# Performance work log

Hardware: AMD Instinct MI355X
Metric: run time of the kernel (lower is better)

## Reference

```python
import jax, jax.numpy as jnp
import numpy as np

H = 2048      # hidden_size
NH = 8        # attention heads
HD = 256      # head_dim (== global_head_dim here)
FFN = 4096
PLD = 256     # hidden_size_per_layer_input
LTOT = 30     # num_hidden_layers of the whole model (PLE projection width)
NL = 15       # layers in this chunk (L0..L14)
W = 512       # sliding-window cache length
CTX = 1024    # full-attention cache length
POS = 100     # current decode position (seq_len == 1)
FULL_LAYERS = (4, 14)
EPS = 1e-6


def _rms(x, w):
    return x * jax.lax.rsqrt(jnp.mean(x * x, axis=-1, keepdims=True) + EPS) * (1.0 + w)


def _rot_half(x):
    x1, x2 = jnp.split(x, 2, axis=-1)
    return jnp.concatenate([-x2, x1], axis=-1)


def _rope(x, cos, sin):
    return x * cos + _rot_half(x) * sin


def setup_inputs():
    key = jax.random.key(0)
    ks = jax.random.split(key, 24)
    f = jnp.float32
    def w(k, shape, s=0.02):
        return jax.random.normal(k, shape, f) * s
    inp = {}
    inp["hidden_states"] = jax.random.normal(ks[0], (1, 1, H), f)
    pos = jnp.arange(CTX)
    inp["causal_mask_full"] = jnp.where(pos <= POS, 0.0, -1e9).astype(f).reshape(1, 1, 1, CTX)
    pw = jnp.arange(W)
    inp["causal_mask_sliding"] = jnp.where((pw <= POS) & (pw > POS - W), 0.0, -1e9).astype(f).reshape(1, 1, 1, W)
    inp["update_mask"] = (pos == POS).astype(f).reshape(1, 1, CTX, 1)
    inp["per_layer_raw"] = jax.random.normal(ks[1], (1, 1, LTOT * PLD), f)
    def rope_tab(base):
        inv = 1.0 / (base ** (jnp.arange(0, HD, 2, dtype=f) / HD))
        ang = POS * inv
        c = jnp.concatenate([jnp.cos(ang), jnp.cos(ang)]).reshape(1, 1, 1, HD)
        s = jnp.concatenate([jnp.sin(ang), jnp.sin(ang)]).reshape(1, 1, 1, HD)
        return c, s
    inp["cos_s"], inp["sin_s"] = rope_tab(10000.0)   # local layers rope_theta
    inp["cos_f"], inp["sin_f"] = rope_tab(1000000.0) # global layers rope_theta
    inp["K_sliding_in"] = jax.random.normal(ks[2], (13, 1, W, HD), f)
    inp["V_sliding_in"] = jax.random.normal(ks[3], (13, 1, W, HD), f)
    inp["K_full_in"] = jax.random.normal(ks[4], (2, 1, CTX, HD), f)
    inp["V_full_in"] = jax.random.normal(ks[5], (2, 1, CTX, HD), f)
    # learned parameters, stacked over the NL chunk layers
    inp["ple_conv_w"] = w(ks[6], (LTOT * PLD, H))   # 1x1 conv kernel of per_layer_model_projection
    inp["ple_norm_w"] = w(ks[7], (PLD,))
    inp["W_ple"] = w(ks[8], (NL, PLD, H))
    inp["Wq"] = w(ks[9], (NL, H, NH * HD))
    inp["Wk"] = w(ks[10], (NL, H, HD))
    inp["Wv"] = w(ks[11], (NL, H, HD))
    inp["Wo"] = w(ks[12], (NL, NH * HD, H))
    inp["w_in"] = w(ks[13], (NL, H))
    inp["w_post"] = w(ks[14], (NL, H))
    inp["w_qn"] = w(ks[15], (NL, HD))
    inp["w_kn"] = w(ks[16], (NL, HD))
    inp["Wg"] = w(ks[17], (NL, H, FFN))
    inp["Wu"] = w(ks[18], (NL, H, FFN))
    inp["Wd"] = w(ks[19], (NL, FFN, H))
    return inp


def _compute_ple(h, per_layer_raw, ple_conv_w, ple_norm_w):
    # 1x1 conv over (1,H,1,S) == matmul over hidden; projection scale = H**-0.5
    proj = jnp.einsum('bsh,ph->bsp', h, ple_conv_w) * (H ** -0.5)   # (1,1,LTOT*PLD)
    pg = proj.reshape(1, LTOT, PLD)
    # layer_norm(cat([x,-x])) with no affine == RMS normalization of x (mean of doubled vec is 0)
    normed = pg * jax.lax.rsqrt(jnp.mean(pg * pg, axis=-1, keepdims=True) + EPS)
    proj_normed = (normed * ple_norm_w).reshape(1, 1, LTOT * PLD)
    return (proj_normed + per_layer_raw) * (2.0 ** -0.5)            # per_layer_input_scale


def reference(hidden_states, causal_mask_full, causal_mask_sliding, update_mask,
              per_layer_raw, cos_s, sin_s, cos_f, sin_f,
              K_sliding_in, V_sliding_in, K_full_in, V_full_in,
              ple_conv_w, ple_norm_w, W_ple,
              Wq, Wk, Wv, Wo, w_in, w_post, w_qn, w_kn, Wg, Wu, Wd):
    h = hidden_states
    ple = _compute_ple(h, per_layer_raw, ple_conv_w, ple_norm_w)
    scale = HD ** -0.5
    um_full = update_mask                  # (1,1,CTX,1)
    um_slide = update_mask[:, :, :W, :]    # (1,1,W,1)
    Ks_out, Vs_out, Kf_out, Vf_out = [], [], [], []
    kv13_k = kv13_v = kv14_k = kv14_v = None
    si = fi = 0
    for l in range(NL):
        is_full = l in FULL_LAYERS
        hn = _rms(h, w_in[l])
        q = (hn @ Wq[l]).reshape(1, 1, NH, HD).transpose(0, 2, 1, 3)  # (1,NH,1,HD)
        k = (hn @ Wk[l]).reshape(1, 1, 1, HD)                         # (1,kv=1,1,HD)
        v = (hn @ Wv[l]).reshape(1, 1, 1, HD)
        q = _rms(q, w_qn[l])
        k = _rms(k, w_kn[l])
        cos, sin = (cos_f, sin_f) if is_full else (cos_s, sin_s)
        q = _rope(q, cos, sin)
        k = _rope(k, cos, sin)
        if is_full:
            K_in, V_in, um, mask = K_full_in[fi][None], V_full_in[fi][None], um_full, causal_mask_full
        else:
            K_in, V_in, um, mask = K_sliding_in[si][None], V_sliding_in[si][None], um_slide, causal_mask_sliding
        K = K_in * (1.0 - um) + k * um     # scatter current token into its cache slot
        V = V_in * (1.0 - um) + v * um
        att = jax.nn.softmax(jnp.einsum('bhqd,bcd->bhqc', q, K[:, 0]) * scale + mask, axis=-1)
        ctx = jnp.einsum('bhqc,bcd->bhqd', att, V[:, 0])              # (1,NH,1,HD)
        h = h + ctx.transpose(0, 2, 1, 3).reshape(1, 1, NH * HD) @ Wo[l]
        hn2 = _rms(h, w_post[l])
        h = h + (jax.nn.gelu(hn2 @ Wg[l], approximate=True) * (hn2 @ Wu[l])) @ Wd[l]
        pli = ple[:, :, l * PLD:(l + 1) * PLD]                        # (1,1,PLD)
        h = h + jax.nn.gelu(pli, approximate=True) @ W_ple[l]
        if is_full:
            Kf_out.append(K[0]); Vf_out.append(V[0])
            if l == 14:
                kv14_k, kv14_v = K, V
            fi += 1
        else:
            Ks_out.append(K[0]); Vs_out.append(V[0])
            if l == 13:
                kv13_k, kv13_v = K, V
            si += 1
    return (h,
            jnp.stack(Ks_out, 0), jnp.stack(Vs_out, 0),
            jnp.stack(Kf_out, 0), jnp.stack(Vf_out, 0),
            ple, kv13_k, kv13_v, kv14_k, kv14_v)
```

## Files before the change

kernel.cpp:

```cpp
#include <hip/hip_runtime.h>
#include <hip/hip_bf16.h>

#define NL 15
#define POS 100
#define NCOL 101
#define EPS 1e-6f

#define O_H    0
#define O_KS   2048
#define SZ_KS  (13*512*256)
#define O_VS   (O_KS + SZ_KS)
#define O_KF   (O_VS + SZ_KS)
#define SZ_KF  (2*1024*256)
#define O_VF   (O_KF + SZ_KF)
#define O_PLE  (O_VF + SZ_KF)
#define O_K13  (O_PLE + 30*256)
#define O_V13  (O_K13 + 512*256)
#define O_K14  (O_V13 + 512*256)
#define O_V14  (O_K14 + 1024*256)

__device__ __forceinline__ float geluf(float x) {
    float x3 = x*x*x;
    return 0.5f*x*(1.f + tanhf(0.7978845608028654f*(x + 0.044715f*x3)));
}

__device__ __forceinline__ float brsum256(float v, float* sred) {
    #pragma unroll
    for (int o=32;o>0;o>>=1) v += __shfl_xor(v,o);
    __syncthreads();
    if ((threadIdx.x&63)==0) sred[threadIdx.x>>6]=v;
    __syncthreads();
    return sred[0]+sred[1]+sred[2]+sred[3];
}
__device__ __forceinline__ float brmax256(float v, float* sred) {
    #pragma unroll
    for (int o=32;o>0;o>>=1) v = fmaxf(v,__shfl_xor(v,o));
    __syncthreads();
    if ((threadIdx.x&63)==0) sred[threadIdx.x>>6]=v;
    __syncthreads();
    return fmaxf(fmaxf(sred[0],sred[1]),fmaxf(sred[2],sred[3]));
}

struct Job {
    const float* W0; const float* W1; const float* W2;
    int N0, N1, N2;
    const float* src0; const float* src1;
    float* out;
    int K; int rows; int ncb; int mode;
};

__global__ __launch_bounds__(256) void gemv_kernel(Job a, Job b, int blocksA) {
    Job j = ((int)blockIdx.x < blocksA) ? a : b;
    int bid = ((int)blockIdx.x < blocksA) ? blockIdx.x : blockIdx.x - blocksA;
    __shared__ float xs[128];
    __shared__ float sred[4];
    int t = threadIdx.x;
    int cb = bid % j.ncb;
    int kc = bid / j.ncb;
    float rs = 1.f;
    if (j.mode == 0) {
        float ss = 0.f;
        for (int i=t;i<j.K;i+=256){ float v=j.src0[i]; ss += v*v; }
        ss = brsum256(ss, sred);
        rs = rsqrtf(ss/(float)j.K + EPS);
    }
    int i0 = kc * j.rows;
    for (int i=t;i<j.rows;i+=256){
        int ii = i0+i; float x;
        if (j.mode==0)      x = j.src0[ii]*rs*(1.f+j.src1[ii]);
        else if (j.mode==1) x = geluf(j.src0[ii])*j.src1[ii];
        else if (j.mode==2) x = geluf(j.src0[ii]);
        else                x = j.src0[ii];
        xs[i] = x;
    }
    __syncthreads();
    int c = cb*1024 + t*4;
    const float* W = nullptr; int lc=0, Nm=0;
    if (c < j.N0) { W=j.W0; lc=c; Nm=j.N0; }
    else if (c < j.N0+j.N1) { W=j.W1; lc=c-j.N0; Nm=j.N1; }
    else if (c < j.N0+j.N1+j.N2) { W=j.W2; lc=c-j.N0-j.N1; Nm=j.N2; }
    if (W) {
        const float* base = W + (size_t)i0*Nm + lc;
        float4 acc = make_float4(0.f,0.f,0.f,0.f);
        for (int r=0;r<j.rows;r++){
            float4 w = *reinterpret_cast<const float4*>(base + (size_t)r*Nm);
            float x = xs[r];
            acc.x += x*w.x; acc.y += x*w.y; acc.z += x*w.z; acc.w += x*w.w;
        }
        atomicAdd(j.out+c+0, acc.x);
        atomicAdd(j.out+c+1, acc.y);
        atomicAdd(j.out+c+2, acc.z);
        atomicAdd(j.out+c+3, acc.w);
    }
}

__global__ __launch_bounds__(256) void ple_conv_kernel(const float* __restrict__ Wc,
        const float* __restrict__ h, float* __restrict__ proj) {
    int wid = threadIdx.x >> 6, lane = threadIdx.x & 63;
    int p = blockIdx.x*4 + wid;
    const float4* wr = reinterpret_cast<const float4*>(Wc + (size_t)p*2048);
    const float4* hr = reinterpret_cast<const float4*>(h);
    float acc = 0.f;
    #pragma unroll
    for (int it=0; it<8; it++){
        int idx = it*64 + lane;
        float4 w = wr[idx], x = hr[idx];
        acc += w.x*x.x + w.y*x.y + w.z*x.z + w.w*x.w;
    }
    #pragma unroll
    for (int o=32;o>0;o>>=1) acc += __shfl_xor(acc,o);
    if (lane==0) proj[p] = acc * 0.022097086912079608f;
}

__global__ __launch_bounds__(256) void ple_fin_kernel(const float* __restrict__ proj,
        const float* __restrict__ normw, const float* __restrict__ raw,
        float* __restrict__ outple) {
    __shared__ float sred[4];
    int g = blockIdx.x, t = threadIdx.x;
    float v = proj[g*256+t];
    float ss = brsum256(v*v, sred);
    float rms = rsqrtf(ss*(1.f/256.f) + EPS);
    outple[g*256+t] = (v*rms*normw[t] + raw[g*256+t]) * 0.7071067811865476f;
}

__global__ __launch_bounds__(256) void attn_kernel(
    const float* __restrict__ qkv,
    const float* __restrict__ wqn, const float* __restrict__ wkn,
    const float* __restrict__ cosv, const float* __restrict__ sinv,
    const float* __restrict__ Kin, const float* __restrict__ Vin,
    float* __restrict__ ctx, float* __restrict__ ksave, float* __restrict__ vsave) {
    __shared__ float qs[256], ksh[256], sc[128], sred[4];
    int t = threadIdx.x, head = blockIdx.x;
    float qv = qkv[head*256+t];
    float ss = brsum256(qv*qv, sred);
    float qn = qv * rsqrtf(ss*(1.f/256.f)+EPS) * (1.f+wqn[t]);
    qs[t]=qn; __syncthreads();
    float qr = qn*cosv[t] + ((t<128)? -qs[t+128] : qs[t-128])*sinv[t];
    __syncthreads(); qs[t]=qr;
    float kv = qkv[2048+t];
    float ks2 = brsum256(kv*kv, sred);
    float kn = kv*rsqrtf(ks2*(1.f/256.f)+EPS)*(1.f+wkn[t]);
    ksh[t]=kn; __syncthreads();
    float kr = kn*cosv[t] + ((t<128)? -ksh[t+128] : ksh[t-128])*sinv[t];
    __syncthreads(); ksh[t]=kr;
    if (head==0){ ksave[t]=kr; vsave[t]=qkv[2304+t]; }
    __syncthreads();
    float score = -1e30f;
    if (t < NCOL) {
        float acc=0.f;
        if (t==POS){
            for (int d=0;d<256;d++) acc += qs[d]*ksh[d];
        } else {
            const float4* kr4 = reinterpret_cast<const float4*>(Kin + (size_t)t*256);
            #pragma unroll 8
            for (int d4=0; d4<64; d4++){
                float4 k4 = kr4[d4];
                acc += qs[d4*4]*k4.x + qs[d4*4+1]*k4.y + qs[d4*4+2]*k4.z + qs[d4*4+3]*k4.w;
            }
        }
        score = acc * 0.0625f;
    }
    float mx = brmax256(score, sred);
    float e = (t<NCOL)? expf(score-mx) : 0.f;
    float s = brsum256(e, sred);
    if (t<128) sc[t] = (t<NCOL)? e/s : 0.f;
    __syncthreads();
    float acc=0.f;
    for (int c=0;c<POS;c++) acc += sc[c]*Vin[(size_t)c*256+t];
    acc += sc[POS]*qkv[2304+t];
    ctx[head*256+t]=acc;
}

__device__ __constant__ int SL_LAYER[13] = {0,1,2,3,5,6,7,8,9,10,11,12,13};

__global__ __launch_bounds__(256) void kv_kernel(
    const float* __restrict__ Ksl, const float* __restrict__ Vsl,
    const float* __restrict__ Kfl, const float* __restrict__ Vfl,
    const float* __restrict__ kall, const float* __restrict__ vall,
    float* __restrict__ out) {
    int wid = threadIdx.x>>6, lane = threadIdx.x&63;
    int row = blockIdx.x*4 + wid;
    const float* src; float* dst;
    if (row < 6656) {
        int s = row>>9, r = row&511;
        dst = out + O_KS + (size_t)row*256;
        src = (r==POS) ? kall + SL_LAYER[s]*256 : Ksl + (size_t)row*256;
    } else if (row < 13312) {
        int idx = row-6656; int s=idx>>9, r=idx&511;
        dst = out + O_VS + (size_t)idx*256;
        src = (r==POS) ? vall + SL_LAYER[s]*256 : Vsl + (size_t)idx*256;
    } else if (row < 15360) {
        int idx = row-13312; int f=idx>>10, r=idx&1023;
        dst = out + O_KF + (size_t)idx*256;
        src = (r==POS) ? kall + (f?14:4)*256 : Kfl + (size_t)idx*256;
    } else if (row < 17408) {
        int idx = row-15360; int f=idx>>10, r=idx&1023;
        dst = out + O_VF + (size_t)idx*256;
        src = (r==POS) ? vall + (f?14:4)*256 : Vfl + (size_t)idx*256;
    } else if (row < 17920) {
        int r = row-17408;
        dst = out + O_K13 + (size_t)r*256;
        src = (r==POS) ? kall + 13*256 : Ksl + (size_t)(12*512+r)*256;
    } else if (row < 18432) {
        int r = row-17920;
        dst = out + O_V13 + (size_t)r*256;
        src = (r==POS) ? vall + 13*256 : Vsl + (size_t)(12*512+r)*256;
    } else if (row < 19456) {
        int r = row-18432;
        dst = out + O_K14 + (size_t)r*256;
        src = (r==POS) ? kall + 14*256 : Kfl + (size_t)(1024+r)*256;
    } else {
        int r = row-19456;
        dst = out + O_V14 + (size_t)r*256;
        src = (r==POS) ? vall + 14*256 : Vfl + (size_t)(1024+r)*256;
    }
    float4 v = reinterpret_cast<const float4*>(src)[lane];
    reinterpret_cast<float4*>(dst)[lane] = v;
}

extern "C" void kernel_launch(void* const* d_in, const int* in_sizes, int n_in,
                              void* d_out, int out_size, void* d_ws, size_t ws_size,
                              hipStream_t stream) {
    const float* hidden = (const float*)d_in[0];
    const float* raw    = (const float*)d_in[4];
    const float* cos_s  = (const float*)d_in[5];
    const float* sin_s  = (const float*)d_in[6];
    const float* cos_f  = (const float*)d_in[7];
    const float* sin_f  = (const float*)d_in[8];
    const float* Ksl    = (const float*)d_in[9];
    const float* Vsl    = (const float*)d_in[10];
    const float* Kfl    = (const float*)d_in[11];
    const float* Vfl    = (const float*)d_in[12];
    const float* ple_conv_w = (const float*)d_in[13];
    const float* ple_norm_w = (const float*)d_in[14];
    const float* W_ple  = (const float*)d_in[15];
    const float* Wq     = (const float*)d_in[16];
    const float* Wk     = (const float*)d_in[17];
    const float* Wv     = (const float*)d_in[18];
    const float* Wo     = (const float*)d_in[19];
    const float* w_in   = (const float*)d_in[20];
    const float* w_post = (const float*)d_in[21];
    const float* w_qn   = (const float*)d_in[22];
    const float* w_kn   = (const float*)d_in[23];
    const float* Wg     = (const float*)d_in[24];
    const float* Wu     = (const float*)d_in[25];
    const float* Wd     = (const float*)d_in[26];
    float* out = (float*)d_out;
    float* ws  = (float*)d_ws;

    float* qkv_all = ws;
    float* gu_all  = ws + 38400;
    float* ctxb    = ws + 161280;
    float* proj    = ws + 163328;
    float* kall    = ws + 171008;
    float* vall    = ws + 174848;

    float* hbuf = out + O_H;
    float* pleb = out + O_PLE;

    hipMemsetAsync(ws, 0, (size_t)161280*4, stream);
    hipMemcpyAsync(hbuf, hidden, 2048*sizeof(float), hipMemcpyDeviceToDevice, stream);
    ple_conv_kernel<<<1920,256,0,stream>>>(ple_conv_w, hbuf, proj);
    ple_fin_kernel<<<30,256,0,stream>>>(proj, ple_norm_w, raw, pleb);

    Job z = {};
    int si=0, fi=0;
    for (int l=0;l<NL;l++){
        bool full = (l==4)||(l==14);
        const float* cv = full? cos_f: cos_s;
        const float* sv = full? sin_f: sin_s;
        const float* Kin = full? Kfl + (size_t)fi*1024*256 : Ksl + (size_t)si*512*256;
        const float* Vin = full? Vfl + (size_t)fi*1024*256 : Vsl + (size_t)si*512*256;
        float* qkv = qkv_all + l*2560;
        float* gu  = gu_all + l*8192;

        Job jq;
        jq.W0 = Wq + (size_t)l*2048*2048; jq.N0 = 2048;
        jq.W1 = Wk + (size_t)l*2048*256;  jq.N1 = 256;
        jq.W2 = Wv + (size_t)l*2048*256;  jq.N2 = 256;
        jq.src0 = hbuf; jq.src1 = w_in + l*2048;
        jq.out = qkv; jq.K = 2048; jq.rows = 32; jq.ncb = 3; jq.mode = 0;
        int gq = 3*(2048/32);
        gemv_kernel<<<gq,256,0,stream>>>(jq, z, gq);

        attn_kernel<<<8,256,0,stream>>>(qkv, w_qn+l*256, w_kn+l*256, cv, sv,
                                        Kin, Vin, ctxb, kall+l*256, vall+l*256);

        Job jo;
        jo.W0 = Wo + (size_t)l*2048*2048; jo.N0=2048; jo.W1=nullptr; jo.N1=0; jo.W2=nullptr; jo.N2=0;
        jo.src0 = ctxb; jo.src1=nullptr; jo.out = hbuf; jo.K=2048; jo.rows=32; jo.ncb=2; jo.mode=3;
        int go = 2*(2048/32);
        gemv_kernel<<<go,256,0,stream>>>(jo, z, go);

        Job jg;
        jg.W0 = Wg + (size_t)l*2048*4096; jg.N0=4096;
        jg.W1 = Wu + (size_t)l*2048*4096; jg.N1=4096; jg.W2=nullptr; jg.N2=0;
        jg.src0=hbuf; jg.src1=w_post+l*2048; jg.out=gu; jg.K=2048; jg.rows=64; jg.ncb=8; jg.mode=0;
        int gg = 8*(2048/64);
        gemv_kernel<<<gg,256,0,stream>>>(jg, z, gg);

        Job jd;
        jd.W0 = Wd + (size_t)l*4096*2048; jd.N0=2048; jd.W1=nullptr; jd.N1=0; jd.W2=nullptr; jd.N2=0;
        jd.src0=gu; jd.src1=gu+4096; jd.out=hbuf; jd.K=4096; jd.rows=32; jd.ncb=2; jd.mode=1;
        int gd = 2*(4096/32);
        Job jp;
        jp.W0 = W_ple + (size_t)l*256*2048; jp.N0=2048; jp.W1=nullptr; jp.N1=0; jp.W2=nullptr; jp.N2=0;
        jp.src0=pleb + l*256; jp.src1=nullptr; jp.out=hbuf; jp.K=256; jp.rows=64; jp.ncb=2; jp.mode=2;
        int gp = 2*(256/64);
        gemv_kernel<<<gd+gp,256,0,stream>>>(jd, jp, gd);

        if (full) fi++; else si++;
    }
    kv_kernel<<<5120,256,0,stream>>>(Ksl, Vsl, Kfl, Vfl, kall, vall, out);
}
```

Baseline: 1.299 ms.

## Restructure decoder into per-op GEMV kernels with wave-level tasks and fused KV copy

Replaces the generic Job-based GEMV with specialized per-projection kernels. Each wave handles a 16 or 32-row by 256-column strip, and the activation vector is staged in LDS once per block. Accumulation uses unsafeAtomicAdd. All per-layer PLE projections are computed up front, and the PLE residual add is folded into the down-projection kernel. The KV cache copy is split across layers and runs inside the attention launch, which also now uses wave-per-column dot products. The intent is more parallelism per GEMV, fewer launches, and the large KV copy overlapping with attention, at the cost of many more atomics on the output buffers.

After: 2.044 ms (median of 2 runs). +57.4%, slower.

```diff
diff --git a/kernel.cpp b/kernel.cpp
--- a/kernel.cpp
+++ b/kernel.cpp
@@ -1,10 +1,12 @@
 #include <hip/hip_runtime.h>
 #include <hip/hip_bf16.h>
 
+#define NT 256
 #define NL 15
 #define POS 100
 #define NCOL 101
 #define EPS 1e-6f
+#define CPB 192
 
 #define O_H    0
 #define O_KS   2048
@@ -19,6 +21,8 @@
 #define O_K14  (O_V13 + 512*256)
 #define O_V14  (O_K14 + 1024*256)
 
+__device__ __forceinline__ void fadd(float* p, float v){ unsafeAtomicAdd(p, v); }
+
 __device__ __forceinline__ float geluf(float x) {
     float x3 = x*x*x;
     return 0.5f*x*(1.f + tanhf(0.7978845608028654f*(x + 0.044715f*x3)));
@@ -41,181 +45,256 @@
     return fmaxf(fmaxf(sred[0],sred[1]),fmaxf(sred[2],sred[3]));
 }
 
-struct Job {
-    const float* W0; const float* W1; const float* W2;
-    int N0, N1, N2;
-    const float* src0; const float* src1;
-    float* out;
-    int K; int rows; int ncb; int mode;
-};
-
-__global__ __launch_bounds__(256) void gemv_kernel(Job a, Job b, int blocksA) {
-    Job j = ((int)blockIdx.x < blocksA) ? a : b;
-    int bid = ((int)blockIdx.x < blocksA) ? blockIdx.x : blockIdx.x - blocksA;
-    __shared__ float xs[128];
-    __shared__ float sred[4];
+template<int MODE>
+__device__ void stage_x(const float* __restrict__ s0, const float* __restrict__ s1,
+                        int K, float* xs, float* sred) {
     int t = threadIdx.x;
-    int cb = bid % j.ncb;
-    int kc = bid / j.ncb;
-    float rs = 1.f;
-    if (j.mode == 0) {
-        float ss = 0.f;
-        for (int i=t;i<j.K;i+=256){ float v=j.src0[i]; ss += v*v; }
-        ss = brsum256(ss, sred);
-        rs = rsqrtf(ss/(float)j.K + EPS);
-    }
-    int i0 = kc * j.rows;
-    for (int i=t;i<j.rows;i+=256){
-        int ii = i0+i; float x;
-        if (j.mode==0)      x = j.src0[ii]*rs*(1.f+j.src1[ii]);
-        else if (j.mode==1) x = geluf(j.src0[ii])*j.src1[ii];
-        else if (j.mode==2) x = geluf(j.src0[ii]);
-        else                x = j.src0[ii];
-        xs[i] = x;
-    }
-    __syncthreads();
-    int c = cb*1024 + t*4;
-    const float* W = nullptr; int lc=0, Nm=0;
-    if (c < j.N0) { W=j.W0; lc=c; Nm=j.N0; }
-    else if (c < j.N0+j.N1) { W=j.W1; lc=c-j.N0; Nm=j.N1; }
-    else if (c < j.N0+j.N1+j.N2) { W=j.W2; lc=c-j.N0-j.N1; Nm=j.N2; }
-    if (W) {
-        const float* base = W + (size_t)i0*Nm + lc;
-        float4 acc = make_float4(0.f,0.f,0.f,0.f);
-        for (int r=0;r<j.rows;r++){
-            float4 w = *reinterpret_cast<const float4*>(base + (size_t)r*Nm);
-            float x = xs[r];
-            acc.x += x*w.x; acc.y += x*w.y; acc.z += x*w.z; acc.w += x*w.w;
+    if (MODE==0){
+        float ss=0.f;
+        for (int i=t;i<K;i+=NT){ float v=s0[i]; xs[i]=v; ss+=v*v; }
+        ss = brsum256(ss,sred);
+        float rs = rsqrtf(ss*(1.f/(float)K)+EPS);
+        for (int i=t;i<K;i+=NT) xs[i] = xs[i]*rs*(1.f+s1[i]);
+    } else if (MODE==1){
+        for (int i=t;i<K;i+=NT) xs[i]=geluf(s0[i])*s0[K+i];
+    } else if (MODE==2){
+        for (int i=t;i<K;i+=NT) xs[i]=geluf(s0[i]);
+    } else {
+        for (int i=t;i<K;i+=NT) xs[i]=s0[i];
+    }
+    __syncthreads();
+}
+
+template<int R>
+__device__ __forceinline__ void gemv4(const float* __restrict__ Wt, int N,
+        const float* __restrict__ xs, float* __restrict__ outc) {
+    int lane = threadIdx.x & 63;
+    float4 acc = make_float4(0.f,0.f,0.f,0.f);
+    #pragma unroll 8
+    for (int r=0;r<R;r++){
+        float x = xs[r];
+        float4 w = *reinterpret_cast<const float4*>(Wt + (size_t)r*N + lane*4);
+        acc.x += x*w.x; acc.y += x*w.y; acc.z += x*w.z; acc.w += x*w.w;
+    }
+    fadd(outc+lane*4+0, acc.x);
+    fadd(outc+lane*4+1, acc.y);
+    fadd(outc+lane*4+2, acc.z);
+    fadd(outc+lane*4+3, acc.w);
+}
+
+__global__ __launch_bounds__(NT) void k_pre(const float* __restrict__ hidden,
+        const float* __restrict__ Wc, float* __restrict__ proj, float* __restrict__ hbuf) {
+    int b=blockIdx.x, t=threadIdx.x, wid=t>>6, lane=t&63;
+    if (b==480){ for (int i=t;i<2048;i+=NT) hbuf[i]=hidden[i]; return; }
+    const float4* hr = reinterpret_cast<const float4*>(hidden);
+    int row0 = b*16 + wid*4;
+    for (int rr=0;rr<4;rr++){
+        int row = row0+rr;
+        const float4* wr = reinterpret_cast<const float4*>(Wc + (size_t)row*2048);
+        float acc=0.f;
+        #pragma unroll
+        for (int it=0; it<8; it++){
+            int idx=it*64+lane;
+            float4 w=wr[idx], x=hr[idx];
+            acc += w.x*x.x + w.y*x.y + w.z*x.z + w.w*x.w;
         }
-        atomicAdd(j.out+c+0, acc.x);
-        atomicAdd(j.out+c+1, acc.y);
-        atomicAdd(j.out+c+2, acc.z);
-        atomicAdd(j.out+c+3, acc.w);
-    }
-}
-
-__global__ __launch_bounds__(256) void ple_conv_kernel(const float* __restrict__ Wc,
-        const float* __restrict__ h, float* __restrict__ proj) {
-    int wid = threadIdx.x >> 6, lane = threadIdx.x & 63;
-    int p = blockIdx.x*4 + wid;
-    const float4* wr = reinterpret_cast<const float4*>(Wc + (size_t)p*2048);
-    const float4* hr = reinterpret_cast<const float4*>(h);
-    float acc = 0.f;
-    #pragma unroll
-    for (int it=0; it<8; it++){
-        int idx = it*64 + lane;
-        float4 w = wr[idx], x = hr[idx];
-        acc += w.x*x.x + w.y*x.y + w.z*x.z + w.w*x.w;
-    }
-    #pragma unroll
-    for (int o=32;o>0;o>>=1) acc += __shfl_xor(acc,o);
-    if (lane==0) proj[p] = acc * 0.022097086912079608f;
-}
-
-__global__ __launch_bounds__(256) void ple_fin_kernel(const float* __restrict__ proj,
-        const float* __restrict__ normw, const float* __restrict__ raw,
-        float* __restrict__ outple) {
-    __shared__ float sred[4];
-    int g = blockIdx.x, t = threadIdx.x;
+        #pragma unroll
+        for (int o=32;o>0;o>>=1) acc += __shfl_xor(acc,o);
+        if (lane==0) proj[row] = acc * 0.022097086912079608f;
+    }
+}
+
+__global__ __launch_bounds__(NT) void k_plef(const float* __restrict__ proj,
+        const float* __restrict__ normw, const float* __restrict__ raw, float* __restrict__ pleb) {
+    __shared__ float sred[8];
+    int g=blockIdx.x, t=threadIdx.x;
     float v = proj[g*256+t];
     float ss = brsum256(v*v, sred);
-    float rms = rsqrtf(ss*(1.f/256.f) + EPS);
-    outple[g*256+t] = (v*rms*normw[t] + raw[g*256+t]) * 0.7071067811865476f;
-}
-
-__global__ __launch_bounds__(256) void attn_kernel(
-    const float* __restrict__ qkv,
-    const float* __restrict__ wqn, const float* __restrict__ wkn,
-    const float* __restrict__ cosv, const float* __restrict__ sinv,
-    const float* __restrict__ Kin, const float* __restrict__ Vin,
-    float* __restrict__ ctx, float* __restrict__ ksave, float* __restrict__ vsave) {
-    __shared__ float qs[256], ksh[256], sc[128], sred[4];
-    int t = threadIdx.x, head = blockIdx.x;
-    float qv = qkv[head*256+t];
+    float rms = rsqrtf(ss*(1.f/256.f)+EPS);
+    pleb[g*256+t] = (v*rms*normw[t] + raw[g*256+t]) * 0.7071067811865476f;
+}
+
+__global__ __launch_bounds__(NT) void k_pleh(const float* __restrict__ pleb,
+        const float* __restrict__ W_ple, float* __restrict__ pleh) {
+    __shared__ float xs[256]; __shared__ float sred[8];
+    int b=blockIdx.x, l=b>>5, wid=threadIdx.x>>6;
+    stage_x<2>(pleb + l*256, nullptr, 256, xs, sred);
+    int task=(b&31)*4+wid;
+    int kc=task&15, strip=task>>4;
+    gemv4<16>(W_ple + (size_t)l*256*2048 + (size_t)kc*16*2048 + strip*256, 2048,
+              xs+kc*16, pleh + l*2048 + strip*256);
+}
+
+__global__ __launch_bounds__(NT) void k_qkv(const float* __restrict__ hbuf,
+        const float* __restrict__ Wq_l, const float* __restrict__ Wk_l,
+        const float* __restrict__ Wv_l, const float* __restrict__ w_in_l,
+        float* __restrict__ qkv) {
+    __shared__ float xs[2048]; __shared__ float sred[8];
+    stage_x<0>(hbuf, w_in_l, 2048, xs, sred);
+    int task = blockIdx.x*4 + (threadIdx.x>>6);
+    if (task < 1024){
+        int strip=task&7, kc=task>>3;
+        gemv4<16>(Wq_l + (size_t)kc*16*2048 + strip*256, 2048, xs+kc*16, qkv + strip*256);
+    } else if (task < 1152){
+        int kc=task-1024;
+        gemv4<16>(Wk_l + (size_t)kc*16*256, 256, xs+kc*16, qkv + 2048);
+    } else {
+        int kc=task-1152;
+        gemv4<16>(Wv_l + (size_t)kc*16*256, 256, xs+kc*16, qkv + 2304);
+    }
+}
+
+__global__ __launch_bounds__(NT) void k_opj(const float* __restrict__ ctx,
+        const float* __restrict__ Wo_l, float* __restrict__ hbuf) {
+    __shared__ float xs[2048]; __shared__ float sred[8];
+    stage_x<3>(ctx, nullptr, 2048, xs, sred);
+    int task = blockIdx.x*4 + (threadIdx.x>>6);
+    int strip=task&7, kc=task>>3;
+    gemv4<16>(Wo_l + (size_t)kc*16*2048 + strip*256, 2048, xs+kc*16, hbuf + strip*256);
+}
+
+__global__ __launch_bounds__(NT) void k_gu(const float* __restrict__ hbuf,
+        const float* __restrict__ Wg_l, const float* __restrict__ Wu_l,
+        const float* __restrict__ w_post_l, float* __restrict__ gu) {
+    __shared__ float xs[2048]; __shared__ float sred[8];
+    stage_x<0>(hbuf, w_post_l, 2048, xs, sred);
+    int task = blockIdx.x*4 + (threadIdx.x>>6);
+    int half = task>>11, tt = task&2047;
+    int strip=tt&15, kc=tt>>4;
+    const float* W = half ? Wu_l : Wg_l;
+    gemv4<16>(W + (size_t)kc*16*4096 + strip*256, 4096, xs+kc*16, gu + half*4096 + strip*256);
+}
+
+__global__ __launch_bounds__(NT, 2) void k_down(const float* __restrict__ gu,
+        const float* __restrict__ Wd_l, const float* __restrict__ pleh_l,
+        float* __restrict__ hbuf) {
+    __shared__ float xs[4096]; __shared__ float sred[8];
+    stage_x<1>(gu, nullptr, 4096, xs, sred);
+    int lane = threadIdx.x & 63;
+    int task = blockIdx.x*4 + (threadIdx.x>>6);
+    if (task < 1024){
+        int strip=task&7, kc=task>>3;
+        gemv4<32>(Wd_l + (size_t)kc*32*2048 + strip*256, 2048, xs+kc*32, hbuf + strip*256);
+    } else if (task < 1032){
+        int base=(task-1024)*256 + lane*4;
+        #pragma unroll
+        for (int j=0;j<4;j++) fadd(hbuf+base+j, pleh_l[base+j]);
+    }
+}
+
+__device__ bool kv_row(float* out, const float* Ksl, const float* Vsl,
+                       const float* Kfl, const float* Vfl,
+                       int row, const float*& src, float*& dst) {
+    if (row < 6656) {
+        int r = row&511; dst = out + O_KS + (size_t)row*256;
+        if (r==POS) return false; src = Ksl + (size_t)row*256;
+    } else if (row < 13312) {
+        int idx = row-6656; int r = idx&511; dst = out + O_VS + (size_t)idx*256;
+        if (r==POS) return false; src = Vsl + (size_t)idx*256;
+    } else if (row < 15360) {
+        int idx = row-13312; int r = idx&1023; dst = out + O_KF + (size_t)idx*256;
+        if (r==POS) return false; src = Kfl + (size_t)idx*256;
+    } else if (row < 17408) {
+        int idx = row-15360; int r = idx&1023; dst = out + O_VF + (size_t)idx*256;
+        if (r==POS) return false; src = Vfl + (size_t)idx*256;
+    } else if (row < 17920) {
+        int r = row-17408; dst = out + O_K13 + (size_t)r*256;
+        if (r==POS) return false; src = Ksl + (size_t)(12*512+r)*256;
+    } else if (row < 18432) {
+        int r = row-17920; dst = out + O_V13 + (size_t)r*256;
+        if (r==POS) return false; src = Vsl + (size_t)(12*512+r)*256;
+    } else if (row < 19456) {
+        int r = row-18432; dst = out + O_K14 + (size_t)r*256;
+        if (r==POS) return false; src = Kfl + (size_t)(1024+r)*256;
+    } else {
+        int r = row-19456; dst = out + O_V14 + (size_t)r*256;
+        if (r==POS) return false; src = Vfl + (size_t)(1024+r)*256;
+    }
+    return true;
+}
+
+__device__ __forceinline__ void writeKpatch(float* out, int l, int t, float v){
+    if (l==4){ out[O_KF + (size_t)POS*256 + t] = v; }
+    else if (l==14){ out[O_KF + (size_t)(1024+POS)*256 + t] = v; out[O_K14 + (size_t)POS*256 + t] = v; }
+    else {
+        int si = l - (l>4 ? 1 : 0);
+        out[O_KS + ((size_t)si*512+POS)*256 + t] = v;
+        if (l==13) out[O_K13 + (size_t)POS*256 + t] = v;
+    }
+}
+__device__ __forceinline__ void writeVpatch(float* out, int l, int t, float v){
+    if (l==4){ out[O_VF + (size_t)POS*256 + t] = v; }
+    else if (l==14){ out[O_VF + (size_t)(1024+POS)*256 + t] = v; out[O_V14 + (size_t)POS*256 + t] = v; }
+    else {
+        int si = l - (l>4 ? 1 : 0);
+        out[O_VS + ((size_t)si*512+POS)*256 + t] = v;
+        if (l==13) out[O_V13 + (size_t)POS*256 + t] = v;
+    }
+}
+
+struct AttnA {
+    const float *qkv, *cosv, *sinv, *Kin, *Vin, *wqn, *wkn;
+    const float *Ksl, *Vsl, *Kfl, *Vfl;
+    float *ctx, *out;
+    int l, r0, r1;
+};
+
+__global__ __launch_bounds__(NT) void k_attn(AttnA a) {
+    __shared__ float qs[256], ksh[256], vsh[256], scb[128], part[1024], sred[8];
+    int bid=blockIdx.x, t=threadIdx.x, wid=t>>6, lane=t&63;
+    if (bid >= 8){
+        for (int r = a.r0 + (bid-8)*4 + wid; r < a.r1; r += CPB*4){
+            const float* s; float* d;
+            if (kv_row(a.out, a.Ksl, a.Vsl, a.Kfl, a.Vfl, r, s, d))
+                reinterpret_cast<float4*>(d)[lane] = reinterpret_cast<const float4*>(s)[lane];
+        }
+        return;
+    }
+    int head = bid;
+    float qv = a.qkv[head*256+t];
     float ss = brsum256(qv*qv, sred);
-    float qn = qv * rsqrtf(ss*(1.f/256.f)+EPS) * (1.f+wqn[t]);
+    float qn = qv * rsqrtf(ss*(1.f/256.f)+EPS) * (1.f+a.wqn[t]);
     qs[t]=qn; __syncthreads();
-    float qr = qn*cosv[t] + ((t<128)? -qs[t+128] : qs[t-128])*sinv[t];
+    float qr = qn*a.cosv[t] + ((t<128)? -qs[t+128] : qs[t-128])*a.sinv[t];
     __syncthreads(); qs[t]=qr;
-    float kv = qkv[2048+t];
+    float kv = a.qkv[2048+t];
     float ks2 = brsum256(kv*kv, sred);
-    float kn = kv*rsqrtf(ks2*(1.f/256.f)+EPS)*(1.f+wkn[t]);
+    float kn = kv*rsqrtf(ks2*(1.f/256.f)+EPS)*(1.f+a.wkn[t]);
     ksh[t]=kn; __syncthreads();
-    float kr = kn*cosv[t] + ((t<128)? -ksh[t+128] : ksh[t-128])*sinv[t];
-    __syncthreads(); ksh[t]=kr;
-    if (head==0){ ksave[t]=kr; vsave[t]=qkv[2304+t]; }
-    __syncthreads();
-    float score = -1e30f;
-    if (t < NCOL) {
-        float acc=0.f;
-        if (t==POS){
-            for (int d=0;d<256;d++) acc += qs[d]*ksh[d];
-        } else {
-            const float4* kr4 = reinterpret_cast<const float4*>(Kin + (size_t)t*256);
-            #pragma unroll 8
-            for (int d4=0; d4<64; d4++){
-                float4 k4 = kr4[d4];
-                acc += qs[d4*4]*k4.x + qs[d4*4+1]*k4.y + qs[d4*4+2]*k4.z + qs[d4*4+3]*k4.w;
-            }
-        }
-        score = acc * 0.0625f;
-    }
+    float kr = kn*a.cosv[t] + ((t<128)? -ksh[t+128] : ksh[t-128])*a.sinv[t];
+    float vr = a.qkv[2304+t];
+    __syncthreads(); ksh[t]=kr; vsh[t]=vr;
+    if (head==0) writeKpatch(a.out, a.l, t, kr);
+    else if (head==1) writeVpatch(a.out, a.l, t, vr);
+    __syncthreads();
+
+    float4 q4 = *reinterpret_cast<const float4*>(qs + lane*4);
+    for (int c=wid; c<NCOL; c+=4){
+        float4 k4 = (c==POS) ? *reinterpret_cast<const float4*>(ksh + lane*4)
+                             : *reinterpret_cast<const float4*>(a.Kin + (size_t)c*256 + lane*4);
+        float d = q4.x*k4.x + q4.y*k4.y + q4.z*k4.z + q4.w*k4.w;
+        #pragma unroll
+        for (int o=32;o>0;o>>=1) d += __shfl_xor(d,o);
+        if (lane==0) scb[c] = d * 0.0625f;
+    }
+    __syncthreads();
+    float score = (t<NCOL) ? scb[t] : -1e30f;
     float mx = brmax256(score, sred);
-    float e = (t<NCOL)? expf(score-mx) : 0.f;
+    float e = (t<NCOL) ? expf(score-mx) : 0.f;
     float s = brsum256(e, sred);
-    if (t<128) sc[t] = (t<NCOL)? e/s : 0.f;
-    __syncthreads();
-    float acc=0.f;
-    for (int c=0;c<POS;c++) acc += sc[c]*Vin[(size_t)c*256+t];
-    acc += sc[POS]*qkv[2304+t];
-    ctx[head*256+t]=acc;
-}
-
-__device__ __constant__ int SL_LAYER[13] = {0,1,2,3,5,6,7,8,9,10,11,12,13};
-
-__global__ __launch_bounds__(256) void kv_kernel(
-    const float* __restrict__ Ksl, const float* __restrict__ Vsl,
-    const float* __restrict__ Kfl, const float* __restrict__ Vfl,
-    const float* __restrict__ kall, const float* __restrict__ vall,
-    float* __restrict__ out) {
-    int wid = threadIdx.x>>6, lane = threadIdx.x&63;
-    int row = blockIdx.x*4 + wid;
-    const float* src; float* dst;
-    if (row < 6656) {
-        int s = row>>9, r = row&511;
-        dst = out + O_KS + (size_t)row*256;
-        src = (r==POS) ? kall + SL_LAYER[s]*256 : Ksl + (size_t)row*256;
-    } else if (row < 13312) {
-        int idx = row-6656; int s=idx>>9, r=idx&511;
-        dst = out + O_VS + (size_t)idx*256;
-        src = (r==POS) ? vall + SL_LAYER[s]*256 : Vsl + (size_t)idx*256;
-    } else if (row < 15360) {
-        int idx = row-13312; int f=idx>>10, r=idx&1023;
-        dst = out + O_KF + (size_t)idx*256;
-        src = (r==POS) ? kall + (f?14:4)*256 : Kfl + (size_t)idx*256;
-    } else if (row < 17408) {
-        int idx = row-15360; int f=idx>>10, r=idx&1023;
-        dst = out + O_VF + (size_t)idx*256;
-        src = (r==POS) ? vall + (f?14:4)*256 : Vfl + (size_t)idx*256;
-    } else if (row < 17920) {
-        int r = row-17408;
-        dst = out + O_K13 + (size_t)r*256;
-        src = (r==POS) ? kall + 13*256 : Ksl + (size_t)(12*512+r)*256;
-    } else if (row < 18432) {
-        int r = row-17920;
-        dst = out + O_V13 + (size_t)r*256;
-        src = (r==POS) ? vall + 13*256 : Vsl + (size_t)(12*512+r)*256;
-    } else if (row < 19456) {
-        int r = row-18432;
-        dst = out + O_K14 + (size_t)r*256;
-        src = (r==POS) ? kall + 14*256 : Kfl + (size_t)(1024+r)*256;
-    } else {
-        int r = row-19456;
-        dst = out + O_V14 + (size_t)r*256;
-        src = (r==POS) ? vall + 14*256 : Vfl + (size_t)(1024+r)*256;
-    }
-    float4 v = reinterpret_cast<const float4*>(src)[lane];
-    reinterpret_cast<float4*>(dst)[lane] = v;
+    if (t<128) scb[t] = (t<NCOL) ? e/s : 0.f;
+    __syncthreads();
+
+    float4 a4 = make_float4(0.f,0.f,0.f,0.f);
+    for (int c=wid; c<NCOL; c+=4){
+        float sc = scb[c];
+        float4 v4 = (c==POS) ? *reinterpret_cast<const float4*>(vsh + lane*4)
+                             : *reinterpret_cast<const float4*>(a.Vin + (size_t)c*256 + lane*4);
+        a4.x += sc*v4.x; a4.y += sc*v4.y; a4.z += sc*v4.z; a4.w += sc*v4.w;
+    }
+    *reinterpret_cast<float4*>(part + wid*256 + lane*4) = a4;
+    __syncthreads();
+    a.ctx[head*256+t] = part[t] + part[256+t] + part[512+t] + part[768+t];
 }
 
 extern "C" void kernel_launch(void* const* d_in, const int* in_sizes, int n_in,
@@ -250,66 +329,43 @@
 
     float* qkv_all = ws;
     float* gu_all  = ws + 38400;
-    float* ctxb    = ws + 161280;
-    float* proj    = ws + 163328;
-    float* kall    = ws + 171008;
-    float* vall    = ws + 174848;
-
-    float* hbuf = out + O_H;
-    float* pleb = out + O_PLE;
-
-    hipMemsetAsync(ws, 0, (size_t)161280*4, stream);
-    hipMemcpyAsync(hbuf, hidden, 2048*sizeof(float), hipMemcpyDeviceToDevice, stream);
-    ple_conv_kernel<<<1920,256,0,stream>>>(ple_conv_w, hbuf, proj);
-    ple_fin_kernel<<<30,256,0,stream>>>(proj, ple_norm_w, raw, pleb);
-
-    Job z = {};
-    int si=0, fi=0;
-    for (int l=0;l<NL;l++){
+    float* pleh    = ws + 161280;
+    float* ctx     = ws + 192000;
+    float* proj    = ws + 194048;
+    float* hbuf    = out + O_H;
+    float* pleb    = out + O_PLE;
+
+    hipMemsetAsync(ws, 0, (size_t)192000*4, stream);
+    k_pre<<<481, NT, 0, stream>>>(hidden, ple_conv_w, proj, hbuf);
+    k_plef<<<30, NT, 0, stream>>>(proj, ple_norm_w, raw, pleb);
+    k_pleh<<<480, NT, 0, stream>>>(pleb, W_ple, pleh);
+    k_qkv<<<320, NT, 0, stream>>>(hbuf, Wq, Wk, Wv, w_in, qkv_all);
+
+    int fi=0, si=0;
+    for (int l=0; l<NL; l++){
         bool full = (l==4)||(l==14);
-        const float* cv = full? cos_f: cos_s;
-        const float* sv = full? sin_f: sin_s;
-        const float* Kin = full? Kfl + (size_t)fi*1024*256 : Ksl + (size_t)si*512*256;
-        const float* Vin = full? Vfl + (size_t)fi*1024*256 : Vsl + (size_t)si*512*256;
-        float* qkv = qkv_all + l*2560;
-        float* gu  = gu_all + l*8192;
-
-        Job jq;
-        jq.W0 = Wq + (size_t)l*2048*2048; jq.N0 = 2048;
-        jq.W1 = Wk + (size_t)l*2048*256;  jq.N1 = 256;
-        jq.W2 = Wv + (size_t)l*2048*256;  jq.N2 = 256;
-        jq.src0 = hbuf; jq.src1 = w_in + l*2048;
-        jq.out = qkv; jq.K = 2048; jq.rows = 32; jq.ncb = 3; jq.mode = 0;
-        int gq = 3*(2048/32);
-        gemv_kernel<<<gq,256,0,stream>>>(jq, z, gq);
-
-        attn_kernel<<<8,256,0,stream>>>(qkv, w_qn+l*256, w_kn+l*256, cv, sv,
-                                        Kin, Vin, ctxb, kall+l*256, vall+l*256);
-
-        Job jo;
-        jo.W0 = Wo + (size_t)l*2048*2048; jo.N0=2048; jo.W1=nullptr; jo.N1=0; jo.W2=nullptr; jo.N2=0;
-        jo.src0 = ctxb; jo.src1=nullptr; jo.out = hbuf; jo.K=2048; jo.rows=32; jo.ncb=2; jo.mode=3;
-        int go = 2*(2048/32);
-        gemv_kernel<<<go,256,0,stream>>>(jo, z, go);
-
-        Job jg;
-        jg.W0 = Wg + (size_t)l*2048*4096; jg.N0=4096;
-        jg.W1 = Wu + (size_t)l*2048*4096; jg.N1=4096; jg.W2=nullptr; jg.N2=0;
-        jg.src0=hbuf; jg.src1=w_post+l*2048; jg.out=gu; jg.K=2048; jg.rows=64; jg.ncb=8; jg.mode=0;
-        int gg = 8*(2048/64);
-        gemv_kernel<<<gg,256,0,stream>>>(jg, z, gg);
-
-        Job jd;
-        jd.W0 = Wd + (size_t)l*4096*2048; jd.N0=2048; jd.W1=nullptr; jd.N1=0; jd.W2=nullptr; jd.N2=0;
-        jd.src0=gu; jd.src1=gu+4096; jd.out=hbuf; jd.K=4096; jd.rows=32; jd.ncb=2; jd.mode=1;
-        int gd = 2*(4096/32);
-        Job jp;
-        jp.W0 = W_ple + (size_t)l*256*2048; jp.N0=2048; jp.W1=nullptr; jp.N1=0; jp.W2=nullptr; jp.N2=0;
-        jp.src0=pleb + l*256; jp.src1=nullptr; jp.out=hbuf; jp.K=256; jp.rows=64; jp.ncb=2; jp.mode=2;
-        int gp = 2*(256/64);
-        gemv_kernel<<<gd+gp,256,0,stream>>>(jd, jp, gd);
-
+        AttnA a;
+        a.qkv = qkv_all + l*2560;
+        a.cosv = full? cos_f : cos_s;  a.sinv = full? sin_f : sin_s;
+        a.Kin  = full? Kfl + (size_t)fi*1024*256 : Ksl + (size_t)si*512*256;
+        a.Vin  = full? Vfl + (size_t)fi*1024*256 : Vsl + (size_t)si*512*256;
+        a.wqn  = w_qn + l*256;  a.wkn = w_kn + l*256;
+        a.Ksl = Ksl; a.Vsl = Vsl; a.Kfl = Kfl; a.Vfl = Vfl;
+        a.ctx = ctx; a.out = out; a.l = l;
+        a.r0 = (20480*l)/15;  a.r1 = (20480*(l+1))/15;
+        k_attn<<<8+CPB, NT, 0, stream>>>(a);
+
+        k_opj<<<256, NT, 0, stream>>>(ctx, Wo + (size_t)l*2048*2048, hbuf);
+        k_gu<<<1024, NT, 0, stream>>>(hbuf, Wg + (size_t)l*2048*4096,
+                                      Wu + (size_t)l*2048*4096, w_post + l*2048,
+                                      gu_all + l*8192);
+        k_down<<<258, NT, 0, stream>>>(gu_all + l*8192, Wd + (size_t)l*4096*2048,
+                                       pleh + l*2048, hbuf);
+        if (l < 14)
+            k_qkv<<<320, NT, 0, stream>>>(hbuf, Wq + (size_t)(l+1)*2048*2048,
+                                          Wk + (size_t)(l+1)*2048*256,
+                                          Wv + (size_t)(l+1)*2048*256,
+                                          w_in + (l+1)*2048, qkv_all + (l+1)*2560);
         if (full) fi++; else si++;
     }
-    kv_kernel<<<5120,256,0,stream>>>(Ksl, Vsl, Kfl, Vfl, kall, vall, out);
-}
+}
```
